# Optimization experiments

Measured on AMD Instinct MI355X. Metric: run time of the kernel, lower is better.

The kernel has to match this reference:

```python
import jax, jax.numpy as jnp
import numpy as np

B, T, D, H, CL = 2, 4096, 2048, 16, 512
DK = D // H          # key_dim == head_dim (value_factor=1) == 128
SCALING = DK ** -0.5


def _rel_pos():
    # RetNet relative position: per-head decay gamma, rotary sin/cos, chunk decay masks
    h = np.arange(H, dtype=np.float64)
    gamma = 1.0 - 2.0 ** (-5.0 - h)                           # (H,)
    angle = 1.0 / (10000.0 ** (np.arange(0, DK, 2) / DK))
    angle = np.repeat(angle, 2)                               # (DK,) each freq duplicated
    pos = np.arange(T)[:, None] * angle[None, :]              # (T, DK)
    sin, cos = np.sin(pos), np.cos(pos)
    idx = np.arange(CL)
    expn = idx[:, None] - idx[None, :]                        # (CL, CL)
    m = np.where(expn >= 0, gamma[:, None, None] ** np.maximum(expn, 0), 0.0)  # (H,CL,CL)
    scale = np.sqrt(m.sum(-1, keepdims=True))                 # (H,CL,1)
    mask = m / scale
    cross_decay = (gamma ** CL)[:, None, None]                # (H,1,1)
    inner = gamma[:, None] ** (idx + 1)                       # (H,CL)
    inner_decay = inner[:, :, None] / (scale / mask[:, -1].sum(-1)[:, None, None])  # (H,CL,1)
    f32 = lambda a: jnp.asarray(a, jnp.float32)
    return f32(sin), f32(cos), f32(mask), f32(cross_decay), f32(inner_decay)


def setup_inputs() -> dict:
    key = jax.random.key(0)
    kx, kq, kk, kv, kg, ko = jax.random.split(key, 6)
    sin, cos, mask, cross_decay, inner_decay = _rel_pos()
    mk = lambda k: jax.random.normal(k, (D, D), jnp.float32) * 0.02  # ~xavier w/ small gain
    z = jnp.zeros((D,), jnp.float32)
    return dict(
        x=jax.random.normal(kx, (B, T, D), jnp.float32),
        sin=sin, cos=cos, mask=mask, cross_decay=cross_decay, inner_decay=inner_decay,
        wq=mk(kq), bq=z, wk=mk(kk), bk=z, wv=mk(kv), bv=z, wg=mk(kg), bg=z,
        wo=jax.random.normal(ko, (D, D), jnp.float32) * (1.0 / np.sqrt(D)), bo=z,
    )


def _rotate_every_two(x):
    x1, x2 = x[..., ::2], x[..., 1::2]
    return jnp.stack((-x2, x1), axis=-1).reshape(x.shape)


def _theta_shift(x, sin, cos):
    return x * cos + _rotate_every_two(x) * sin


def reference(x, sin, cos, mask, cross_decay, inner_decay,
              wq, bq, wk, bk, wv, bv, wg, bg, wo, bo):
    NC = T // CL
    q = (x @ wq.T + bq).reshape(B, T, H, DK).transpose(0, 2, 1, 3)           # (B,H,T,DK)
    k = ((x @ wk.T + bk) * SCALING).reshape(B, T, H, DK).transpose(0, 2, 1, 3)
    v = x @ wv.T + bv                                                        # (B,T,D)
    g = x @ wg.T + bg
    qr = _theta_shift(q, sin, cos)
    kr = _theta_shift(k, sin, cos)
    # chunk views -> (B, NC, H, CL, DK)
    qr = qr.reshape(B, H, NC, CL, DK).transpose(0, 2, 1, 3, 4)
    kr = kr.reshape(B, H, NC, CL, DK).transpose(0, 2, 1, 3, 4)
    vc = v.reshape(B, NC, CL, H, DK).transpose(0, 1, 3, 2, 4)                # (B,NC,H,CL,HD)
    # intra-chunk decay-masked attention
    qk = jnp.einsum('bnhld,bnhmd->bnhlm', qr, kr) * mask                      # (B,NC,H,CL,CL)
    inner_scale = jnp.clip(jnp.abs(jax.lax.stop_gradient(qk)).sum(-1, keepdims=True), 1.0)
    inner_out = jnp.einsum('bnhlm,bnhmd->bnhld', qk / inner_scale, vc)
    # per-chunk KV contribution (keys weighted by remaining decay = last mask row)
    kv = jnp.einsum('bnhlk,bnhld->bnhkd', kr, vc * mask[:, -1, :, None])      # (B,NC,H,DK,HD)

    def step(carry, kv_i):
        kv_state, kv_scale = carry
        out = (kv_state / kv_scale, kv_scale)
        new_state = kv_state * cross_decay + kv_i
        s = jnp.abs(jax.lax.stop_gradient(new_state)).sum(-2, keepdims=True)
        new_scale = jnp.clip(s.max(-1, keepdims=True), 1.0)
        return (new_state, new_scale), out

    init = (jnp.zeros((B, H, DK, DK), x.dtype), jnp.ones((B, H, 1, 1), x.dtype))
    _, (kv_rec, cross_scale) = jax.lax.scan(step, init, jnp.moveaxis(kv, 1, 0))
    kv_rec = jnp.moveaxis(kv_rec, 0, 1)            # (B,NC,H,DK,HD)
    cross_scale = jnp.moveaxis(cross_scale, 0, 1)  # (B,NC,H,1,1)
    all_scale = jnp.maximum(inner_scale, cross_scale)
    cross_out = jnp.einsum('bnhlk,bnhkd->bnhld', qr * inner_decay, kv_rec)
    out = inner_out / (all_scale / inner_scale) + cross_out / (all_scale / cross_scale)
    out = out.transpose(0, 1, 3, 2, 4)             # (B,NC,CL,H,HD)
    # group_norm: LayerNorm over head_dim, no affine, eps=1e-6
    mu = out.mean(-1, keepdims=True)
    var = ((out - mu) ** 2).mean(-1, keepdims=True)
    out = (out - mu) / jnp.sqrt(var + 1e-6)
    out = out.reshape(B, T, D)
    out = jax.nn.silu(g) * out                     # swish gate
    return out @ wo.T + bo
```

## Files before the change

### kernel.cpp

```cpp
#include <hip/hip_runtime.h>
#include <hip/hip_bf16.h>
#include <math.h>

#define NB   2
#define NT   4096
#define ND   2048
#define NH   16
#define NDK  128
#define NCL  512
#define NNC  8
#define NTOK 8192
#define SCALING 0.08838834764831845f

typedef unsigned short u16;
typedef short short8 __attribute__((ext_vector_type(8)));
typedef unsigned short ushort8 __attribute__((ext_vector_type(8)));
typedef float f32x4 __attribute__((ext_vector_type(4)));
typedef float float4v __attribute__((ext_vector_type(4)));
typedef short short4v __attribute__((ext_vector_type(4)));

__device__ __forceinline__ float bf2f(u16 u) {
    union { unsigned int i; float f; } v; v.i = ((unsigned int)u) << 16; return v.f;
}
__device__ __forceinline__ u16 f2bf(float f) {
    union { float f; unsigned int i; } v; v.f = f;
    unsigned int r = v.i + 0x7FFFu + ((v.i >> 16) & 1u);
    return (u16)(r >> 16);
}

__device__ __forceinline__ void gload16(const void* g, void* l) {
    __builtin_amdgcn_global_load_lds(
        (const __attribute__((address_space(1))) unsigned int*)g,
        (__attribute__((address_space(3))) unsigned int*)l, 16, 0, 0);
}

#define MFMA16(acc_, a_, b_) acc_ = __builtin_amdgcn_mfma_f32_16x16x32_bf16(a_, b_, acc_, 0, 0, 0)
#define SBAR  asm volatile("s_barrier" ::: "memory")


__device__ __forceinline__ void stage_half(const u16* __restrict__ g, int ld,
                                           u16* lds, int tid)
{
#pragma unroll
    for (int j = 0; j < 2; ++j) {
        int c = tid + j * 512;
        int row = c >> 3, u = c & 7;
        gload16(g + (size_t)row * ld + ((u ^ (row & 7)) * 8), lds + (size_t)c * 8);
    }
}

__device__ __forceinline__ void tile4(
    int G, int nkt,
    const u16* __restrict__ Aop, const u16* __restrict__ Bop,
    int lda, int ldb, int tid, int arow, int brow, int uc0, int uc1,
    u16* ARd, u16* BRd, u16* AWr, u16* BWr,
    f32x4 acc[8][4])
{
    short8 a[4][2], bA[2][2], bB[2][2];

#pragma unroll
    for (int mf = 0; mf < 4; ++mf) {
        a[mf][0] = *(const short8*)(ARd + (size_t)(arow + mf * 16) * 64 + uc0);
        a[mf][1] = *(const short8*)(ARd + (size_t)(arow + mf * 16) * 64 + uc1);
    }
#pragma unroll
    for (int nf = 0; nf < 2; ++nf) {
        bA[nf][0] = *(const short8*)(BRd + (size_t)(brow + nf * 16) * 64 + uc0);
        bA[nf][1] = *(const short8*)(BRd + (size_t)(brow + nf * 16) * 64 + uc1);
    }
    if (G + 1 < nkt)
        stage_half(Aop + (size_t)128 * lda + (size_t)(G + 1) * 64, lda, AWr + 8192, tid);
    SBAR;
    __builtin_amdgcn_s_setprio(1);
#pragma unroll
    for (int mf = 0; mf < 4; ++mf)
#pragma unroll
        for (int nf = 0; nf < 2; ++nf) {
            MFMA16(acc[mf][nf], a[mf][0], bA[nf][0]);
            MFMA16(acc[mf][nf], a[mf][1], bA[nf][1]);
        }
    __builtin_amdgcn_s_setprio(0);
    SBAR;

#pragma unroll
    for (int nf = 0; nf < 2; ++nf) {
        bB[nf][0] = *(const short8*)(BRd + (size_t)(brow + 32 + nf * 16) * 64 + uc0);
        bB[nf][1] = *(const short8*)(BRd + (size_t)(brow + 32 + nf * 16) * 64 + uc1);
    }
    SBAR;
    __builtin_amdgcn_s_setprio(1);
#pragma unroll
    for (int mf = 0; mf < 4; ++mf)
#pragma unroll
        for (int nf = 0; nf < 2; ++nf) {
            MFMA16(acc[mf][2 + nf], a[mf][0], bB[nf][0]);
            MFMA16(acc[mf][2 + nf], a[mf][1], bB[nf][1]);
        }
    __builtin_amdgcn_s_setprio(0);
    SBAR;

#pragma unroll
    for (int mf = 0; mf < 4; ++mf) {
        a[mf][0] = *(const short8*)(ARd + (size_t)(arow + 64 + mf * 16) * 64 + uc0);
        a[mf][1] = *(const short8*)(ARd + (size_t)(arow + 64 + mf * 16) * 64 + uc1);
    }
    if (G + 2 < nkt)
        stage_half(Bop + (size_t)(G + 2) * 64, ldb, BRd, tid);
    SBAR;
    __builtin_amdgcn_s_setprio(1);
#pragma unroll
    for (int mf = 0; mf < 4; ++mf)
#pragma unroll
        for (int nf = 0; nf < 2; ++nf) {
            MFMA16(acc[4 + mf][2 + nf], a[mf][0], bB[nf][0]);
            MFMA16(acc[4 + mf][2 + nf], a[mf][1], bB[nf][1]);
        }
    __builtin_amdgcn_s_setprio(0);
    SBAR;

    if (G + 2 < nkt) {
        stage_half(Bop + (size_t)128 * ldb + (size_t)(G + 2) * 64, ldb, BRd + 8192, tid);
        stage_half(Aop + (size_t)(G + 2) * 64, lda, ARd, tid);
        asm volatile("s_waitcnt vmcnt(6)" ::: "memory");
    } else if (G + 1 < nkt) {
        asm volatile("s_waitcnt vmcnt(0)" ::: "memory");
    }
    SBAR;
    __builtin_amdgcn_s_setprio(1);
#pragma unroll
    for (int mf = 0; mf < 4; ++mf)
#pragma unroll
        for (int nf = 0; nf < 2; ++nf) {
            MFMA16(acc[4 + mf][nf], a[mf][0], bA[nf][0]);
            MFMA16(acc[4 + mf][nf], a[mf][1], bA[nf][1]);
        }
    __builtin_amdgcn_s_setprio(0);
    SBAR;
}

__device__ __forceinline__ void gemm256_core(
    const u16* __restrict__ Aop, const u16* __restrict__ Bop,
    int lda, int ldb, int nkt,
    u16* A0, u16* A1, u16* B0, u16* B1, f32x4 acc[8][4])
{
    const int tid  = threadIdx.x;
    const int lane = tid & 63;
    const int lr   = lane & 15;
    const int lg   = lane >> 4;
    const int wid  = tid >> 6;
    const int wm   = wid >> 2;
    const int wn   = wid & 3;

    const int swz  = lr & 7;
    const int uc0  = ((0 * 4 + lg) ^ swz) * 8;
    const int uc1  = ((1 * 4 + lg) ^ swz) * 8;
    const int arow = wm * 128 + lr;
    const int brow = wn * 64 + lr;

    stage_half(Bop,                       ldb, B0,        tid);
    stage_half(Bop + (size_t)128 * ldb,   ldb, B0 + 8192, tid);
    stage_half(Aop,                       lda, A0,        tid);
    stage_half(Aop + (size_t)128 * lda,   lda, A0 + 8192, tid);
    stage_half(Bop + 64,                     ldb, B1,        tid);
    stage_half(Bop + (size_t)128 * ldb + 64, ldb, B1 + 8192, tid);
    stage_half(Aop + 64,                     lda, A1,        tid);
    asm volatile("s_waitcnt vmcnt(6)" ::: "memory");
    SBAR;

    for (int G = 0; G < nkt; G += 2) {
        tile4(G,     nkt, Aop, Bop, lda, ldb, tid, arow, brow, uc0, uc1,
              A0, B0, A1, B1, acc);
        tile4(G + 1, nkt, Aop, Bop, lda, ldb, tid, arow, brow, uc0, uc1,
              A1, B1, A0, B0, acc);
    }
}

__device__ __forceinline__ void gemm_bt_core(
    const u16* __restrict__ A, const u16* __restrict__ Bm,
    int lda, int ldb, int K, u16* As, u16* Bs, f32x4 acc[4][4])
{
    const int tid  = threadIdx.x;
    const int lane = tid & 63;
    const int lr   = lane & 15;
    const int lg   = lane >> 4;
    const int wid  = tid >> 6;
    const int wr   = (wid >> 1) * 64;
    const int wc   = (wid & 1) * 64;
    for (int kt = 0; kt < K; kt += 64) {
#pragma unroll
        for (int i = 0; i < 4; ++i) {
            int c = tid + i * 256;
            int row = c >> 3, col = (c & 7) * 8;
            gload16(A  + (size_t)row * lda + kt + col, (char*)As + (size_t)c * 16);
            gload16(Bm + (size_t)row * ldb + kt + col, (char*)Bs + (size_t)c * 16);
        }
        __syncthreads();
#pragma unroll
        for (int kk = 0; kk < 2; ++kk) {
            short8 a[4], b[4];
#pragma unroll
            for (int m = 0; m < 4; ++m)
                a[m] = *(const short8*)(As + (wr + m * 16 + lr) * 64 + kk * 32 + lg * 8);
#pragma unroll
            for (int n = 0; n < 4; ++n)
                b[n] = *(const short8*)(Bs + (wc + n * 16 + lr) * 64 + kk * 32 + lg * 8);
#pragma unroll
            for (int m = 0; m < 4; ++m)
#pragma unroll
                for (int n = 0; n < 4; ++n)
                    acc[m][n] = __builtin_amdgcn_mfma_f32_16x16x32_bf16(a[m], b[n], acc[m][n], 0, 0, 0);
        }
        __syncthreads();
    }
}

__global__ __launch_bounds__(256) void k_f2bf(const float* __restrict__ src,
                                              u16* __restrict__ dst, int n4)
{
    int i = blockIdx.x * blockDim.x + threadIdx.x;
    int stride = gridDim.x * blockDim.x;
    for (int j = i; j < n4; j += stride) {
        float4v f = *(const float4v*)(src + (size_t)j * 4);
        short4v o;
        o.x = (short)f2bf(f.x); o.y = (short)f2bf(f.y);
        o.z = (short)f2bf(f.z); o.w = (short)f2bf(f.w);
        *(short4v*)(dst + (size_t)j * 4) = o;
    }
}

__global__ __launch_bounds__(512, 2) void k_gemm1(
    const u16* __restrict__ xb, const u16* __restrict__ wb,
    const float* __restrict__ bq, const float* __restrict__ bk,
    const float* __restrict__ bv, const float* __restrict__ bg,
    const float* __restrict__ sinp, const float* __restrict__ cosp,
    const float* __restrict__ maskp,
    u16* __restrict__ qro, u16* __restrict__ kro, u16* __restrict__ krwT,
    u16* __restrict__ vT, u16* __restrict__ glin)
{
    __shared__ __align__(16) u16 A0[256 * 64];
    __shared__ __align__(16) u16 A1[256 * 64];
    __shared__ __align__(16) u16 B0[256 * 64];
    __shared__ __align__(16) u16 B1[256 * 64];
    f32x4 acc[8][4];
#pragma unroll
    for (int m = 0; m < 8; ++m)
#pragma unroll
        for (int n = 0; n < 4; ++n) acc[m][n] = (f32x4){0.f, 0.f, 0.f, 0.f};

    int bid = blockIdx.x;
    int swzb = (bid & 7) * 128 + (bid >> 3);
    int mt = swzb >> 5, nt = swzb & 31;

    gemm256_core(xb + (size_t)mt * 256 * ND, wb + (size_t)nt * 256 * ND,
                 ND, ND, ND / 64, A0, A1, B0, B1, acc);

    int tid = threadIdx.x, lane = tid & 63, lr = lane & 15, lg = lane >> 4, wid = tid >> 6;
    int wm = wid >> 2, wn = wid & 3;
    int which = nt >> 3;

    if (which <= 1) {
        const float* bias = (which == 0) ? bq : bk;
#pragma unroll
        for (int mf = 0; mf < 8; ++mf) {
#pragma unroll
            for (int nf = 0; nf < 4; ++nf) {
#pragma unroll
                for (int r = 0; r < 4; ++r) {
                    int row = mt * 256 + wm * 128 + mf * 16 + lg * 4 + r;
                    int col = nt * 256 + wn * 64 + nf * 16 + lr;
                    int f = col & 2047, h = f >> 7, d = f & 127;
                    int b = row >> 12, t = row & 4095, cn = t >> 9, cl = t & 511;
                    float v = acc[mf][nf][r] + bias[f];
                    if (which == 1) v *= SCALING;
                    float sv = sinp[(size_t)t * NDK + d];
                    float cv = cosp[(size_t)t * NDK + d];
                    float vp = __shfl_xor(v, 1);
                    float rot = (lr & 1) ? vp : -vp;
                    float o = v * cv + rot * sv;
                    size_t chbase = (size_t)(b * NNC + cn) * NH + h;
                    if (which == 0) {
                        qro[(chbase * NCL + cl) * NDK + d] = f2bf(o);
                    } else {
                        kro[(chbase * NCL + cl) * NDK + d] = f2bf(o);
                        float w = maskp[((size_t)h * NCL + (NCL - 1)) * NCL + cl];
                        krwT[(chbase * NDK + d) * NCL + cl] = f2bf(o * w);
                    }
                }
            }
        }
    } else {
#pragma unroll
        for (int mf = 0; mf < 8; ++mf) {
#pragma unroll
            for (int nf = 0; nf < 4; ++nf) {
#pragma unroll
                for (int r = 0; r < 4; ++r) {
                    int row = mt * 256 + wm * 128 + mf * 16 + lg * 4 + r;
                    int col = nt * 256 + wn * 64 + nf * 16 + lr;
                    int f = col & 2047;
                    float v = acc[mf][nf][r];
                    if (which == 2) {
                        int h = f >> 7, d = f & 127;
                        int b = row >> 12, t = row & 4095, cn = t >> 9, cl = t & 511;
                        vT[(((size_t)(b * NNC + cn) * NH + h) * NDK + d) * NCL + cl] = f2bf(v + bv[f]);
                    } else {
                        glin[(size_t)row * ND + f] = f2bf(v + bg[f]);
                    }
                }
            }
        }
    }
}

__global__ __launch_bounds__(512, 2) void k_gemm2(
    const u16* __restrict__ y, const u16* __restrict__ wob,
    const float* __restrict__ bo, float* __restrict__ out)
{
    __shared__ __align__(16) u16 A0[256 * 64];
    __shared__ __align__(16) u16 A1[256 * 64];
    __shared__ __align__(16) u16 B0[256 * 64];
    __shared__ __align__(16) u16 B1[256 * 64];
    f32x4 acc[8][4];
#pragma unroll
    for (int m = 0; m < 8; ++m)
#pragma unroll
        for (int n = 0; n < 4; ++n) acc[m][n] = (f32x4){0.f, 0.f, 0.f, 0.f};

    int bid = blockIdx.x;
    int swzb = (bid & 7) * 32 + (bid >> 3);
    int mt = swzb >> 3, nt = swzb & 7;

    gemm256_core(y + (size_t)mt * 256 * ND, wob + (size_t)nt * 256 * ND,
                 ND, ND, ND / 64, A0, A1, B0, B1, acc);

    int tid = threadIdx.x, lane = tid & 63, lr = lane & 15, lg = lane >> 4, wid = tid >> 6;
    int wm = wid >> 2, wn = wid & 3;
#pragma unroll
    for (int mf = 0; mf < 8; ++mf)
#pragma unroll
        for (int nf = 0; nf < 4; ++nf)
#pragma unroll
            for (int r = 0; r < 4; ++r) {
                int row = mt * 256 + wm * 128 + mf * 16 + lg * 4 + r;
                int col = nt * 256 + wn * 64 + nf * 16 + lr;
                out[(size_t)row * ND + col] = acc[mf][nf][r] + bo[col];
            }
}

__global__ __launch_bounds__(256) void k_inner(
    const u16* __restrict__ qr, const u16* __restrict__ kr,
    const u16* __restrict__ vT, const float* __restrict__ mask,
    float* __restrict__ iraw, float* __restrict__ iscale)
{
    __shared__ __align__(16) u16 Qs[128 * 128];
    __shared__ __align__(16) u16 Ks[32 * 128];
    __shared__ __align__(16) u16 Vs[128 * 32];
    __shared__ __align__(16) u16 Ps[4][32 * 32];
    __shared__ float sl[128];

    int qt = blockIdx.x, bnh = blockIdx.y;
    int h = bnh & 15;
    const u16* Q = qr + (size_t)bnh * NCL * NDK + (size_t)qt * 128 * NDK;
    const u16* K = kr + (size_t)bnh * NCL * NDK;
    const u16* V = vT + (size_t)bnh * NDK * NCL;
    const float* M = mask + (size_t)h * NCL * NCL + (size_t)qt * 128 * NCL;

    int tid = threadIdx.x, lane = tid & 63, lr = lane & 15, lg = lane >> 4, wid = tid >> 6;
    if (tid < 128) sl[tid] = 0.f;
#pragma unroll
    for (int i = 0; i < 8; ++i) {
        int c = tid + i * 256;
        gload16(Q + (size_t)c * 8, (char*)Qs + (size_t)c * 16);
    }
    __syncthreads();

    short8 aq[2][4];
#pragma unroll
    for (int i = 0; i < 2; ++i)
#pragma unroll
        for (int kk = 0; kk < 4; ++kk)
            aq[i][kk] = *(const short8*)(Qs + (wid * 32 + i * 16 + lr) * 128 + kk * 32 + lg * 8);

    f32x4 acc[2][8];
#pragma unroll
    for (int i = 0; i < 2; ++i)
#pragma unroll
        for (int n = 0; n < 8; ++n) acc[i][n] = (f32x4){0.f, 0.f, 0.f, 0.f};

    int msteps = qt * 4 + 4;
    for (int ms = 0; ms < msteps; ++ms) {
        int mb = ms * 32;
#pragma unroll
        for (int i = 0; i < 2; ++i) {
            int c = tid + i * 256;
            int row = c >> 4, cc = (c & 15) * 8;
            gload16(K + (size_t)(mb + row) * NDK + cc, (char*)Ks + (size_t)c * 16);
        }
#pragma unroll
        for (int i = 0; i < 2; ++i) {
            int c = tid + i * 256;
            int row = c >> 2, cc = (c & 3) * 8;
            gload16(V + (size_t)row * NCL + mb + cc, (char*)Vs + (size_t)c * 16);
        }
        __syncthreads();

        f32x4 pa[2][2];
#pragma unroll
        for (int i = 0; i < 2; ++i) { pa[i][0] = (f32x4){0.f,0.f,0.f,0.f}; pa[i][1] = (f32x4){0.f,0.f,0.f,0.f}; }
#pragma unroll
        for (int kk = 0; kk < 4; ++kk) {
            short8 bk0 = *(const short8*)(Ks + (lr) * 128 + kk * 32 + lg * 8);
            short8 bk1 = *(const short8*)(Ks + (16 + lr) * 128 + kk * 32 + lg * 8);
#pragma unroll
            for (int i = 0; i < 2; ++i) {
                pa[i][0] = __builtin_amdgcn_mfma_f32_16x16x32_bf16(aq[i][kk], bk0, pa[i][0], 0, 0, 0);
                pa[i][1] = __builtin_amdgcn_mfma_f32_16x16x32_bf16(aq[i][kk], bk1, pa[i][1], 0, 0, 0);
            }
        }
#pragma unroll
        for (int i = 0; i < 2; ++i) {
#pragma unroll
            for (int r = 0; r < 4; ++r) {
                int rloc = i * 16 + lg * 4 + r;
                int row128 = wid * 32 + rloc;
                float m0 = M[(size_t)row128 * NCL + mb + lr];
                float m1 = M[(size_t)row128 * NCL + mb + 16 + lr];
                float p0 = pa[i][0][r] * m0;
                float p1 = pa[i][1][r] * m1;
                float ss = fabsf(p0) + fabsf(p1);
                ss += __shfl_xor(ss, 1); ss += __shfl_xor(ss, 2);
                ss += __shfl_xor(ss, 4); ss += __shfl_xor(ss, 8);
                if (lr == 0) sl[row128] += ss;
                Ps[wid][rloc * 32 + lr]      = f2bf(p0);
                Ps[wid][rloc * 32 + 16 + lr] = f2bf(p1);
            }
        }
        __syncthreads();

        short8 ap[2];
#pragma unroll
        for (int i = 0; i < 2; ++i)
            ap[i] = *(const short8*)(Ps[wid] + (i * 16 + lr) * 32 + lg * 8);
#pragma unroll
        for (int n = 0; n < 8; ++n) {
            short8 bv8 = *(const short8*)(Vs + (n * 16 + lr) * 32 + lg * 8);
#pragma unroll
            for (int i = 0; i < 2; ++i)
                acc[i][n] = __builtin_amdgcn_mfma_f32_16x16x32_bf16(ap[i], bv8, acc[i][n], 0, 0, 0);
        }
        __syncthreads();
    }

    float* OR = iraw + ((size_t)bnh * NCL + (size_t)qt * 128) * NDK;
#pragma unroll
    for (int i = 0; i < 2; ++i)
#pragma unroll
        for (int n = 0; n < 8; ++n)
#pragma unroll
            for (int r = 0; r < 4; ++r) {
                int row = wid * 32 + i * 16 + lg * 4 + r;
                int col = n * 16 + lr;
                OR[(size_t)row * NDK + col] = acc[i][n][r];
            }
    __syncthreads();
    if (tid < 128) iscale[(size_t)bnh * NCL + qt * 128 + tid] = fmaxf(1.f, sl[tid]);
}

__global__ __launch_bounds__(256) void k_kv(
    const u16* __restrict__ krwT, const u16* __restrict__ vT, float* __restrict__ kvi)
{
    __shared__ __align__(16) u16 As[128 * 64];
    __shared__ __align__(16) u16 Bs[128 * 64];
    f32x4 acc[4][4];
#pragma unroll
    for (int m = 0; m < 4; ++m)
#pragma unroll
        for (int n = 0; n < 4; ++n) acc[m][n] = (f32x4){0.f, 0.f, 0.f, 0.f};

    int bnh = blockIdx.x;
    gemm_bt_core(krwT + (size_t)bnh * NDK * NCL, vT + (size_t)bnh * NDK * NCL,
                 NCL, NCL, NCL, As, Bs, acc);

    int tid = threadIdx.x, lane = tid & 63, lr = lane & 15, lg = lane >> 4, wid = tid >> 6;
    int wr = (wid >> 1) * 64, wc = (wid & 1) * 64;
    float* O = kvi + (size_t)bnh * NDK * NDK;
#pragma unroll
    for (int m = 0; m < 4; ++m)
#pragma unroll
        for (int n = 0; n < 4; ++n)
#pragma unroll
            for (int r = 0; r < 4; ++r) {
                int row = wr + m * 16 + lg * 4 + r;
                int col = wc + n * 16 + lr;
                O[(size_t)row * NDK + col] = acc[m][n][r];
            }
}

__global__ __launch_bounds__(256) void k_scan(
    const float* __restrict__ kvi, const float* __restrict__ cdec,
    u16* __restrict__ kvrT, float* __restrict__ csc)
{
    int bh = blockIdx.x;
    int b = bh >> 4, h = bh & 15;
    float cd = cdec[h];
    int tid = threadIdx.x;
    int col = tid & 127;
    int r0 = (tid >> 7) * 64;
    float st[64];
#pragma unroll
    for (int i = 0; i < 64; ++i) st[i] = 0.f;
    float scale = 1.f;
    __shared__ float cs[128];
    __shared__ float scsh;

    for (int n = 0; n < NNC; ++n) {
        size_t idx = (size_t)((b * NNC + n) * NH + h);
        size_t kb = idx * (NDK * NDK);
        float inv = 1.f / scale;
#pragma unroll
        for (int i = 0; i < 64; ++i)
            kvrT[kb + (size_t)col * NDK + r0 + i] = f2bf(st[i] * inv);
        if (tid == 0) csc[idx] = scale;

        const float* KV = kvi + kb;
        float colsum = 0.f;
#pragma unroll
        for (int i = 0; i < 64; ++i) {
            float xv = st[i] * cd + KV[(size_t)(r0 + i) * NDK + col];
            st[i] = xv;
            colsum += fabsf(xv);
        }
        __syncthreads();
        if (tid < 128) cs[tid] = 0.f;
        __syncthreads();
        atomicAdd(&cs[col], colsum);
        __syncthreads();
        if (tid == 0) {
            float mx = cs[0];
            for (int i = 1; i < 128; ++i) mx = fmaxf(mx, cs[i]);
            scsh = fmaxf(1.f, mx);
        }
        __syncthreads();
        scale = scsh;
    }
}

__global__ __launch_bounds__(256) void k_combine(
    const u16* __restrict__ qr, const u16* __restrict__ kvrT,
    const float* __restrict__ iraw, const float* __restrict__ iscale,
    const float* __restrict__ cscale, const float* __restrict__ idecay,
    const u16* __restrict__ glin, u16* __restrict__ y)
{
    __shared__ __align__(16) u16 As[128 * 64];
    __shared__ __align__(16) u16 Bs[128 * 64];
    __shared__ float ssum[128];
    __shared__ float ssq[128];
    f32x4 acc[4][4];
#pragma unroll
    for (int m = 0; m < 4; ++m)
#pragma unroll
        for (int n = 0; n < 4; ++n) acc[m][n] = (f32x4){0.f, 0.f, 0.f, 0.f};

    int qt = blockIdx.x, bnh = blockIdx.y;
    int b = bnh >> 7, cn = (bnh >> 4) & 7, h = bnh & 15;
    gemm_bt_core(qr + (size_t)bnh * NCL * NDK + (size_t)qt * 128 * NDK,
                 kvrT + (size_t)bnh * NDK * NDK, NDK, NDK, NDK, As, Bs, acc);

    int tid = threadIdx.x, lane = tid & 63, lr = lane & 15, lg = lane >> 4, wid = tid >> 6;
    int wr = (wid >> 1) * 64, wc = (wid & 1) * 64;
    if (tid < 128) { ssum[tid] = 0.f; ssq[tid] = 0.f; }
    __syncthreads();
    float csv = cscale[bnh];

#pragma unroll
    for (int m = 0; m < 4; ++m) {
#pragma unroll
        for (int r = 0; r < 4; ++r) {
            int rloc = wr + m * 16 + lg * 4 + r;
            int l = qt * 128 + rloc;
            float isc = iscale[(size_t)bnh * NCL + l];
            float all = fmaxf(isc, csv);
            float c1 = 1.f / all;
            float c2 = (csv / all) * idecay[h * NCL + l];
            const float* ir = iraw + ((size_t)bnh * NCL + l) * NDK;
            float lsum = 0.f, lsq = 0.f;
#pragma unroll
            for (int n = 0; n < 4; ++n) {
                int col = wc + n * 16 + lr;
                float v = ir[col] * c1 + acc[m][n][r] * c2;
                acc[m][n][r] = v;
                lsum += v; lsq += v * v;
            }
            lsum += __shfl_xor(lsum, 1); lsum += __shfl_xor(lsum, 2);
            lsum += __shfl_xor(lsum, 4); lsum += __shfl_xor(lsum, 8);
            lsq  += __shfl_xor(lsq, 1);  lsq  += __shfl_xor(lsq, 2);
            lsq  += __shfl_xor(lsq, 4);  lsq  += __shfl_xor(lsq, 8);
            if (lr == 0) { atomicAdd(&ssum[rloc], lsum); atomicAdd(&ssq[rloc], lsq); }
        }
    }
    __syncthreads();
#pragma unroll
    for (int m = 0; m < 4; ++m) {
#pragma unroll
        for (int r = 0; r < 4; ++r) {
            int rloc = wr + m * 16 + lg * 4 + r;
            int l = qt * 128 + rloc;
            float mu = ssum[rloc] * (1.f / 128.f);
            float var = ssq[rloc] * (1.f / 128.f) - mu * mu;
            float rstd = rsqrtf(fmaxf(var, 0.f) + 1e-6f);
            int t = cn * NCL + l;
            size_t obase = ((size_t)(b * NT + t)) * ND + (size_t)h * NDK;
#pragma unroll
            for (int n = 0; n < 4; ++n) {
                int col = wc + n * 16 + lr;
                float gv = bf2f(glin[obase + col]);
                float sg = gv / (1.f + expf(-gv));
                float ov = (acc[m][n][r] - mu) * rstd * sg;
                y[obase + col] = f2bf(ov);
            }
        }
    }
}

extern "C" void kernel_launch(void* const* d_in, const int* in_sizes, int n_in,
                              void* d_out, int out_size, void* d_ws, size_t ws_size,
                              hipStream_t stream)
{
    const float* x    = (const float*)d_in[0];
    const float* sinp = (const float*)d_in[1];
    const float* cosp = (const float*)d_in[2];
    const float* mask = (const float*)d_in[3];
    const float* cdec = (const float*)d_in[4];
    const float* idec = (const float*)d_in[5];
    const float* wq   = (const float*)d_in[6];
    const float* bq   = (const float*)d_in[7];
    const float* wk   = (const float*)d_in[8];
    const float* bk   = (const float*)d_in[9];
    const float* wv   = (const float*)d_in[10];
    const float* bv   = (const float*)d_in[11];
    const float* wg   = (const float*)d_in[12];
    const float* bg   = (const float*)d_in[13];
    const float* wo   = (const float*)d_in[14];
    const float* bo   = (const float*)d_in[15];
    float* out = (float*)d_out;

    char* ws = (char*)d_ws;
    u16*   XB   = (u16*)(ws + 0);
    u16*   WB   = (u16*)(ws + 33554432);
    u16*   WOB  = (u16*)(ws + 67108864);
    u16*   QR   = (u16*)(ws + 75497472);
    u16*   KR   = (u16*)(ws + 109051904);
    u16*   KRWT = (u16*)(ws + 142606336);
    u16*   VT   = (u16*)(ws + 176160768);
    u16*   GLIN = (u16*)(ws + 209715200);
    float* KVI  = (float*)(ws + 243269632);
    float* CSC  = (float*)(ws + 260046848);
    float* IRAW = (float*)(ws + 0);
    u16*   Y    = KR;
    u16*   KVRT = KRWT;
    float* ISC  = (float*)(ws + 243269632);

    k_f2bf<<<2048, 256, 0, stream>>>(x, XB, 4194304);
    k_f2bf<<<1024, 256, 0, stream>>>(wq, WB,            1048576);
    k_f2bf<<<1024, 256, 0, stream>>>(wk, WB + 4194304,  1048576);
    k_f2bf<<<1024, 256, 0, stream>>>(wv, WB + 8388608,  1048576);
    k_f2bf<<<1024, 256, 0, stream>>>(wg, WB + 12582912, 1048576);
    k_f2bf<<<1024, 256, 0, stream>>>(wo, WOB,           1048576);

    k_gemm1<<<1024, 512, 0, stream>>>(XB, WB, bq, bk, bv, bg, sinp, cosp, mask,
                                      QR, KR, KRWT, VT, GLIN);
    k_kv<<<256, 256, 0, stream>>>(KRWT, VT, KVI);
    k_scan<<<32, 256, 0, stream>>>(KVI, cdec, KVRT, CSC);
    k_inner<<<dim3(4, 256), 256, 0, stream>>>(QR, KR, VT, mask, IRAW, ISC);
    k_combine<<<dim3(4, 256), 256, 0, stream>>>(QR, KVRT, IRAW, ISC, CSC, idec, GLIN, Y);
    k_gemm2<<<256, 512, 0, stream>>>(Y, WOB, bo, out);
}
```

Baseline: 900.2 us.

## Replace direct global-to-LDS loads with register-staged prefetch in GEMM core

```diff
diff --git a/kernel.cpp b/kernel.cpp
--- a/kernel.cpp
+++ b/kernel.cpp
@@ -38,25 +38,17 @@
 #define SBAR  asm volatile("s_barrier" ::: "memory")
 
 
-__device__ __forceinline__ void stage_half(const u16* __restrict__ g, int ld,
-                                           u16* lds, int tid)
-{
-#pragma unroll
-    for (int j = 0; j < 2; ++j) {
-        int c = tid + j * 512;
-        int row = c >> 3, u = c & 7;
-        gload16(g + (size_t)row * ld + ((u ^ (row & 7)) * 8), lds + (size_t)c * 8);
-    }
-}
-
 __device__ __forceinline__ void tile4(
     int G, int nkt,
-    const u16* __restrict__ Aop, const u16* __restrict__ Bop,
-    int lda, int ldb, int tid, int arow, int brow, int uc0, int uc1,
+    const u16* Aop, const u16* Bop,
+    const size_t* off, const int* lof,
+    int arow, int brow, int uc0, int uc1,
     u16* ARd, u16* BRd, u16* AWr, u16* BWr,
     f32x4 acc[8][4])
 {
     short8 a[4][2], bA[2][2], bB[2][2];
+    int4 ra[4], rb[4];
+    const bool pf = (G + 1 < nkt);
 
 #pragma unroll
     for (int mf = 0; mf < 4; ++mf) {
@@ -68,8 +60,14 @@
         bA[nf][0] = *(const short8*)(BRd + (size_t)(brow + nf * 16) * 64 + uc0);
         bA[nf][1] = *(const short8*)(BRd + (size_t)(brow + nf * 16) * 64 + uc1);
     }
-    if (G + 1 < nkt)
-        stage_half(Aop + (size_t)128 * lda + (size_t)(G + 1) * 64, lda, AWr + 8192, tid);
+    if (pf) {
+        const u16* Ag = Aop + (size_t)(G + 1) * 64;
+        const u16* Bg = Bop + (size_t)(G + 1) * 64;
+#pragma unroll
+        for (int j = 0; j < 4; ++j) ra[j] = *(const int4*)(Ag + off[j]);
+#pragma unroll
+        for (int j = 0; j < 4; ++j) rb[j] = *(const int4*)(Bg + off[j]);
+    }
     SBAR;
     __builtin_amdgcn_s_setprio(1);
 #pragma unroll
@@ -104,8 +102,10 @@
         a[mf][0] = *(const short8*)(ARd + (size_t)(arow + 64 + mf * 16) * 64 + uc0);
         a[mf][1] = *(const short8*)(ARd + (size_t)(arow + 64 + mf * 16) * 64 + uc1);
     }
-    if (G + 2 < nkt)
-        stage_half(Bop + (size_t)(G + 2) * 64, ldb, BRd, tid);
+    if (pf) {
+#pragma unroll
+        for (int j = 0; j < 4; ++j) *(int4*)((char*)AWr + lof[j]) = ra[j];
+    }
     SBAR;
     __builtin_amdgcn_s_setprio(1);
 #pragma unroll
@@ -118,12 +118,10 @@
     __builtin_amdgcn_s_setprio(0);
     SBAR;
 
-    if (G + 2 < nkt) {
-        stage_half(Bop + (size_t)128 * ldb + (size_t)(G + 2) * 64, ldb, BRd + 8192, tid);
-        stage_half(Aop + (size_t)(G + 2) * 64, lda, ARd, tid);
-        asm volatile("s_waitcnt vmcnt(6)" ::: "memory");
-    } else if (G + 1 < nkt) {
-        asm volatile("s_waitcnt vmcnt(0)" ::: "memory");
+    if (pf) {
+#pragma unroll
+        for (int j = 0; j < 4; ++j) *(int4*)((char*)BWr + lof[j]) = rb[j];
+        asm volatile("s_waitcnt lgkmcnt(0)" ::: "memory");
     }
     SBAR;
     __builtin_amdgcn_s_setprio(1);
@@ -139,8 +137,8 @@
 }
 
 __device__ __forceinline__ void gemm256_core(
-    const u16* __restrict__ Aop, const u16* __restrict__ Bop,
-    int lda, int ldb, int nkt,
+    const u16* Aop, const u16* Bop,
+    int ld, int nkt,
     u16* A0, u16* A1, u16* B0, u16* B1, f32x4 acc[8][4])
 {
     const int tid  = threadIdx.x;
@@ -157,20 +155,35 @@
     const int arow = wm * 128 + lr;
     const int brow = wn * 64 + lr;
 
-    stage_half(Bop,                       ldb, B0,        tid);
-    stage_half(Bop + (size_t)128 * ldb,   ldb, B0 + 8192, tid);
-    stage_half(Aop,                       lda, A0,        tid);
-    stage_half(Aop + (size_t)128 * lda,   lda, A0 + 8192, tid);
-    stage_half(Bop + 64,                     ldb, B1,        tid);
-    stage_half(Bop + (size_t)128 * ldb + 64, ldb, B1 + 8192, tid);
-    stage_half(Aop + 64,                     lda, A1,        tid);
-    asm volatile("s_waitcnt vmcnt(6)" ::: "memory");
-    SBAR;
+    size_t off[4];
+    int lof[4];
+#pragma unroll
+    for (int j = 0; j < 4; ++j) {
+        int c = tid + (j & 1) * 512;
+        int row = c >> 3, u = c & 7;
+        int h = j >> 1;
+        off[j] = (size_t)(h * 128 + row) * ld + ((u ^ (row & 7)) * 8);
+        lof[j] = h * 16384 + c * 16;
+    }
+
+    {
+        int4 ta[4], tb[4];
+#pragma unroll
+        for (int j = 0; j < 4; ++j) ta[j] = *(const int4*)(Aop + off[j]);
+#pragma unroll
+        for (int j = 0; j < 4; ++j) tb[j] = *(const int4*)(Bop + off[j]);
+#pragma unroll
+        for (int j = 0; j < 4; ++j) *(int4*)((char*)A0 + lof[j]) = ta[j];
+#pragma unroll
+        for (int j = 0; j < 4; ++j) *(int4*)((char*)B0 + lof[j]) = tb[j];
+        asm volatile("s_waitcnt lgkmcnt(0)" ::: "memory");
+        SBAR;
+    }
 
     for (int G = 0; G < nkt; G += 2) {
-        tile4(G,     nkt, Aop, Bop, lda, ldb, tid, arow, brow, uc0, uc1,
+        tile4(G,     nkt, Aop, Bop, off, lof, arow, brow, uc0, uc1,
               A0, B0, A1, B1, acc);
-        tile4(G + 1, nkt, Aop, Bop, lda, ldb, tid, arow, brow, uc0, uc1,
+        tile4(G + 1, nkt, Aop, Bop, off, lof, arow, brow, uc0, uc1,
               A1, B1, A0, B0, acc);
     }
 }
@@ -252,7 +265,7 @@
     int mt = swzb >> 5, nt = swzb & 31;
 
     gemm256_core(xb + (size_t)mt * 256 * ND, wb + (size_t)nt * 256 * ND,
-                 ND, ND, ND / 64, A0, A1, B0, B1, acc);
+                 ND, ND / 64, A0, A1, B0, B1, acc);
 
     int tid = threadIdx.x, lane = tid & 63, lr = lane & 15, lg = lane >> 4, wid = tid >> 6;
     int wm = wid >> 2, wn = wid & 3;
@@ -331,7 +344,7 @@
     int mt = swzb >> 3, nt = swzb & 7;
 
     gemm256_core(y + (size_t)mt * 256 * ND, wob + (size_t)nt * 256 * ND,
-                 ND, ND, ND / 64, A0, A1, B0, B1, acc);
+                 ND, ND / 64, A0, A1, B0, B1, acc);
 
     int tid = threadIdx.x, lane = tid & 63, lr = lane & 15, lg = lane >> 4, wid = tid >> 6;
     int wm = wid >> 2, wn = wid & 3;
```

Measured after the change: 1.214 ms. +34.9%, slower.

## Simplify GEMM main loop to whole-tile double buffering with one barrier

Applied to the files above, without the earlier changes.

```diff
diff --git a/kernel.cpp b/kernel.cpp
--- a/kernel.cpp
+++ b/kernel.cpp
@@ -49,13 +49,22 @@
     }
 }
 
-__device__ __forceinline__ void tile4(
+__device__ __forceinline__ void tile_nb(
     int G, int nkt,
-    const u16* __restrict__ Aop, const u16* __restrict__ Bop,
-    int lda, int ldb, int tid, int arow, int brow, int uc0, int uc1,
+    const u16* Aop, const u16* Bop, int ld,
+    int tid, int arow, int brow, int uc0, int uc1,
     u16* ARd, u16* BRd, u16* AWr, u16* BWr,
     f32x4 acc[8][4])
 {
+    if (G + 1 < nkt) {
+        const u16* Ag = Aop + (size_t)(G + 1) * 64;
+        const u16* Bg = Bop + (size_t)(G + 1) * 64;
+        stage_half(Ag,                    ld, AWr,        tid);
+        stage_half(Ag + (size_t)128 * ld, ld, AWr + 8192, tid);
+        stage_half(Bg,                    ld, BWr,        tid);
+        stage_half(Bg + (size_t)128 * ld, ld, BWr + 8192, tid);
+    }
+
     short8 a[4][2], bA[2][2], bB[2][2];
 
 #pragma unroll
@@ -68,9 +77,6 @@
         bA[nf][0] = *(const short8*)(BRd + (size_t)(brow + nf * 16) * 64 + uc0);
         bA[nf][1] = *(const short8*)(BRd + (size_t)(brow + nf * 16) * 64 + uc1);
     }
-    if (G + 1 < nkt)
-        stage_half(Aop + (size_t)128 * lda + (size_t)(G + 1) * 64, lda, AWr + 8192, tid);
-    SBAR;
     __builtin_amdgcn_s_setprio(1);
 #pragma unroll
     for (int mf = 0; mf < 4; ++mf)
@@ -80,14 +86,12 @@
             MFMA16(acc[mf][nf], a[mf][1], bA[nf][1]);
         }
     __builtin_amdgcn_s_setprio(0);
-    SBAR;
 
 #pragma unroll
     for (int nf = 0; nf < 2; ++nf) {
         bB[nf][0] = *(const short8*)(BRd + (size_t)(brow + 32 + nf * 16) * 64 + uc0);
         bB[nf][1] = *(const short8*)(BRd + (size_t)(brow + 32 + nf * 16) * 64 + uc1);
     }
-    SBAR;
     __builtin_amdgcn_s_setprio(1);
 #pragma unroll
     for (int mf = 0; mf < 4; ++mf)
@@ -97,16 +101,12 @@
             MFMA16(acc[mf][2 + nf], a[mf][1], bB[nf][1]);
         }
     __builtin_amdgcn_s_setprio(0);
-    SBAR;
 
 #pragma unroll
     for (int mf = 0; mf < 4; ++mf) {
         a[mf][0] = *(const short8*)(ARd + (size_t)(arow + 64 + mf * 16) * 64 + uc0);
         a[mf][1] = *(const short8*)(ARd + (size_t)(arow + 64 + mf * 16) * 64 + uc1);
     }
-    if (G + 2 < nkt)
-        stage_half(Bop + (size_t)(G + 2) * 64, ldb, BRd, tid);
-    SBAR;
     __builtin_amdgcn_s_setprio(1);
 #pragma unroll
     for (int mf = 0; mf < 4; ++mf)
@@ -116,16 +116,7 @@
             MFMA16(acc[4 + mf][2 + nf], a[mf][1], bB[nf][1]);
         }
     __builtin_amdgcn_s_setprio(0);
-    SBAR;
-
-    if (G + 2 < nkt) {
-        stage_half(Bop + (size_t)128 * ldb + (size_t)(G + 2) * 64, ldb, BRd + 8192, tid);
-        stage_half(Aop + (size_t)(G + 2) * 64, lda, ARd, tid);
-        asm volatile("s_waitcnt vmcnt(6)" ::: "memory");
-    } else if (G + 1 < nkt) {
-        asm volatile("s_waitcnt vmcnt(0)" ::: "memory");
-    }
-    SBAR;
+
     __builtin_amdgcn_s_setprio(1);
 #pragma unroll
     for (int mf = 0; mf < 4; ++mf)
@@ -135,12 +126,14 @@
             MFMA16(acc[4 + mf][nf], a[mf][1], bA[nf][1]);
         }
     __builtin_amdgcn_s_setprio(0);
+
+    asm volatile("s_waitcnt vmcnt(0) lgkmcnt(0)" ::: "memory");
     SBAR;
 }
 
 __device__ __forceinline__ void gemm256_core(
-    const u16* __restrict__ Aop, const u16* __restrict__ Bop,
-    int lda, int ldb, int nkt,
+    const u16* Aop, const u16* Bop,
+    int ld, int nkt,
     u16* A0, u16* A1, u16* B0, u16* B1, f32x4 acc[8][4])
 {
     const int tid  = threadIdx.x;
@@ -157,21 +150,18 @@
     const int arow = wm * 128 + lr;
     const int brow = wn * 64 + lr;
 
-    stage_half(Bop,                       ldb, B0,        tid);
-    stage_half(Bop + (size_t)128 * ldb,   ldb, B0 + 8192, tid);
-    stage_half(Aop,                       lda, A0,        tid);
-    stage_half(Aop + (size_t)128 * lda,   lda, A0 + 8192, tid);
-    stage_half(Bop + 64,                     ldb, B1,        tid);
-    stage_half(Bop + (size_t)128 * ldb + 64, ldb, B1 + 8192, tid);
-    stage_half(Aop + 64,                     lda, A1,        tid);
-    asm volatile("s_waitcnt vmcnt(6)" ::: "memory");
+    stage_half(Aop,                    ld, A0,        tid);
+    stage_half(Aop + (size_t)128 * ld, ld, A0 + 8192, tid);
+    stage_half(Bop,                    ld, B0,        tid);
+    stage_half(Bop + (size_t)128 * ld, ld, B0 + 8192, tid);
+    asm volatile("s_waitcnt vmcnt(0)" ::: "memory");
     SBAR;
 
     for (int G = 0; G < nkt; G += 2) {
-        tile4(G,     nkt, Aop, Bop, lda, ldb, tid, arow, brow, uc0, uc1,
-              A0, B0, A1, B1, acc);
-        tile4(G + 1, nkt, Aop, Bop, lda, ldb, tid, arow, brow, uc0, uc1,
-              A1, B1, A0, B0, acc);
+        tile_nb(G,     nkt, Aop, Bop, ld, tid, arow, brow, uc0, uc1,
+                A0, B0, A1, B1, acc);
+        tile_nb(G + 1, nkt, Aop, Bop, ld, tid, arow, brow, uc0, uc1,
+                A1, B1, A0, B0, acc);
     }
 }
 
@@ -252,7 +242,7 @@
     int mt = swzb >> 5, nt = swzb & 31;
 
     gemm256_core(xb + (size_t)mt * 256 * ND, wb + (size_t)nt * 256 * ND,
-                 ND, ND, ND / 64, A0, A1, B0, B1, acc);
+                 ND, ND / 64, A0, A1, B0, B1, acc);
 
     int tid = threadIdx.x, lane = tid & 63, lr = lane & 15, lg = lane >> 4, wid = tid >> 6;
     int wm = wid >> 2, wn = wid & 3;
@@ -331,7 +321,7 @@
     int mt = swzb >> 3, nt = swzb & 7;
 
     gemm256_core(y + (size_t)mt * 256 * ND, wob + (size_t)nt * 256 * ND,
-                 ND, ND, ND / 64, A0, A1, B0, B1, acc);
+                 ND, ND / 64, A0, A1, B0, B1, acc);
 
     int tid = threadIdx.x, lane = tid & 63, lr = lane & 15, lg = lane >> 4, wid = tid >> 6;
     int wm = wid >> 2, wn = wid & 3;
```

Result: faster. 878.0 us (-2.5%).
